# Kernel tuning notes

Measured on AMD Instinct MI355X. Metric: run time of the kernel, lower is better.

Reference implementation:

```python
import jax, jax.numpy as jnp
import numpy as np


def setup_inputs() -> dict:
    key = jax.random.key(0)
    k1, k2 = jax.random.split(key)
    b, feat = 8192, 256
    x = jax.random.normal(k1, (b, feat), dtype=jnp.float32)
    y = jax.random.randint(k2, (b,), 0, 100, dtype=jnp.int64)
    T = jnp.zeros((1,), dtype=jnp.float32)
    return {"x": x, "y": y, "T": T}


def reference(x, y, T):
    # SNNLoss.forward with inv=False, d=None, and no -1 labels in y
    b = x.shape[0]
    x = x / jnp.std(x, ddof=1)  # torch .std() is unbiased (ddof=1)

    # Pairwise Euclidean distance via Gram matrix (avoids [b,b,feat] blowup)
    sq = jnp.sum(x * x, axis=1)  # [b]
    d2 = jnp.maximum(sq[:, None] + sq[None, :] - 2.0 * (x @ x.T), 0.0)  # [b,b]
    eye = jnp.eye(b, dtype=bool)
    # diagonal is exactly 0 and masked out later; keep sqrt grad-safe there
    dist = jnp.where(eye, 0.0, jnp.sqrt(jnp.where(eye, 1.0, d2)))

    e_dist = -dist * jnp.power(jnp.float32(10.0), T[0])  # [b,b]
    neg_inf = jnp.float32(-jnp.inf)

    # denominator: all pairs except self
    den_dist = jnp.where(eye, neg_inf, e_dist)
    den = jax.scipy.special.logsumexp(den_dist, axis=1)  # [b]

    # numerator: same-label pairs except self
    m_num = (y[:, None] == y[None, :]) & ~eye  # [b,b]
    has = jnp.any(m_num, axis=1)  # rows with at least one positive
    num_dist = jnp.where(m_num, e_dist, neg_inf)
    # rows with no positives would give logsumexp = -inf; torch code zeroes
    # both num and den there. Substitute finite values, then zero the term.
    num = jax.scipy.special.logsumexp(jnp.where(has[:, None], num_dist, 0.0), axis=1)
    terms = jnp.where(has, num - den, 0.0)
    return -jnp.mean(terms)
```

## Files before the change

### kernel.cpp

```cpp
#include <hip/hip_runtime.h>

#define B_ROWS 8192
#define FEAT   256
#define NCH    8
#define CH_COLS 1024
#define NJT    16

typedef float f32x4 __attribute__((ext_vector_type(4)));
typedef _Float16 f16x8 __attribute__((ext_vector_type(8)));

typedef const __attribute__((address_space(1))) unsigned int* gas_ptr;
typedef __attribute__((address_space(3))) unsigned int* las_ptr;

__device__ __forceinline__ void gload_lds16(const void* g, void* l) {
  __builtin_amdgcn_global_load_lds((gas_ptr)g, (las_ptr)l, 16, 0, 0);
}

__global__ __launch_bounds__(256) void prep_kernel(
    const float* __restrict__ x, unsigned short* __restrict__ xh,
    float* __restrict__ sq, float* __restrict__ part_s,
    float* __restrict__ part_q)
{
  int tid = threadIdx.x;
  int l = tid & 63, wid = tid >> 6;
  int row = blockIdx.x * 4 + wid;
  const float4* xv = (const float4*)(x + (size_t)row * FEAT);
  float4 v = xv[l];
  ushort4 u;
  u.x = __builtin_bit_cast(unsigned short, (_Float16)v.x);
  u.y = __builtin_bit_cast(unsigned short, (_Float16)v.y);
  u.z = __builtin_bit_cast(unsigned short, (_Float16)v.z);
  u.w = __builtin_bit_cast(unsigned short, (_Float16)v.w);
  ((ushort4*)(xh + (size_t)row * FEAT))[l] = u;
  float ssq  = v.x*v.x + v.y*v.y + v.z*v.z + v.w*v.w;
  float ssum = v.x + v.y + v.z + v.w;
  #pragma unroll
  for (int m = 32; m; m >>= 1) {
    ssq  += __shfl_xor(ssq, m);
    ssum += __shfl_xor(ssum, m);
  }
  if (l == 0) sq[row] = ssq;
  __shared__ float red[8];
  if (l == 0) { red[wid*2] = ssum; red[wid*2+1] = ssq; }
  __syncthreads();
  if (tid == 0) {
    part_s[blockIdx.x] = red[0]+red[2]+red[4]+red[6];
    part_q[blockIdx.x] = red[1]+red[3]+red[5]+red[7];
  }
}

template<bool DIAG>
__device__ __forceinline__ void epilogue(
    const f32x4 (&acc)[2][4], const float* __restrict__ sq,
    const int* __restrict__ y, int j0, int l15,
    int i0q, const float (&sqi)[8], const int (&yiv)[8],
    float (&sden)[8], float (&snum)[8], float nscale2)
{
  int jb = j0 + l15;
  float sqj[4]; int yj[4];
  #pragma unroll
  for (int cb = 0; cb < 4; ++cb) {
    int j = jb + cb*16;
    sqj[cb] = sq[j];
    yj[cb]  = y[j];
  }
  #pragma unroll
  for (int rb = 0; rb < 2; ++rb) {
    #pragma unroll
    for (int r = 0; r < 4; ++r) {
      float si = sqi[rb*4+r];
      int   ig = i0q + rb*16 + r;
      int   yi = yiv[rb*4+r];
      float dacc = 0.f, nacc = 0.f;
      #pragma unroll
      for (int cb = 0; cb < 4; ++cb) {
        float S  = acc[rb][cb][r];
        float d2 = fmaf(S, -2.0f, si + sqj[cb]);
        d2 = fmaxf(d2, 0.0f);
        float e  = __builtin_amdgcn_exp2f(__builtin_amdgcn_sqrtf(d2) * nscale2);
        bool offd = !DIAG || (ig != jb + cb*16);
        dacc += offd ? e : 0.0f;
        nacc += (yi == yj[cb] && offd) ? e : 0.0f;
      }
      sden[rb*4+r] += dacc;
      snum[rb*4+r] += nacc;
    }
  }
}

__global__ __launch_bounds__(256, 2) void snn_main(
    const unsigned short* __restrict__ xh, const float* __restrict__ sq,
    const int* __restrict__ y, const float* __restrict__ T,
    const float* __restrict__ part_s, const float* __restrict__ part_q,
    float* __restrict__ pden, float* __restrict__ pnum)
{
  __shared__ __align__(16) char lB[32768];
  int tid = threadIdx.x;
  int l = tid & 63, wid = tid >> 6;
  int quad = l >> 4, l15 = l & 15;
  int l5 = l >> 5, s31 = l & 31;
  int ch = blockIdx.x, it = blockIdx.y;
  int i0 = it * 128, chbase = ch * CH_COLS;
  const char* xbc = (const char*)xh;

  f16x8 areg[2][8];
  #pragma unroll
  for (int rb = 0; rb < 2; ++rb)
    #pragma unroll
    for (int kk = 0; kk < 8; ++kk)
      areg[rb][kk] = *(const f16x8*)(xbc +
          (size_t)(i0 + wid*32 + rb*16 + l15)*512 + kk*64 + quad*16);

  float s_acc = 0.f, q_acc = 0.f;
  #pragma unroll
  for (int t = 0; t < 32; ++t) {
    s_acc += part_s[l + 64*t];
    q_acc += part_q[l + 64*t];
  }
  #pragma unroll
  for (int m = 1; m <= 32; m <<= 1) {
    s_acc += __shfl_xor(s_acc, m);
    q_acc += __shfl_xor(q_acc, m);
  }
  const double n = (double)B_ROWS * FEAT;
  double var = ((double)q_acc - (double)s_acc*(double)s_acc/n) / (n - 1.0);
  float stdv = (float)sqrt(var);
  float p10  = __builtin_amdgcn_exp2f(T[0] * 3.3219280948873623f);
  float nscale2 = -(p10 * 1.4426950408889634f / stdv);

  float sqi[8]; int yiv[8];
  int i0q = i0 + wid*32 + quad*4;
  #pragma unroll
  for (int rb = 0; rb < 2; ++rb)
    #pragma unroll
    for (int r = 0; r < 4; ++r) {
      int idx = i0q + rb*16 + r;
      sqi[rb*4+r] = sq[idx];
      yiv[rb*4+r] = y[idx];
    }

  float sden[8], snum[8];
  #pragma unroll
  for (int v = 0; v < 8; ++v) { sden[v] = 0.f; snum[v] = 0.f; }
  f32x4 acc[2][4];
  const f32x4 zero4 = {0.f, 0.f, 0.f, 0.f};

  for (int jt = 0; jt < NJT; ++jt) {
    int j0 = chbase + jt * 64;

    __syncthreads();
    {
      const char* gB = xbc + (size_t)j0 * 512;
      #pragma unroll
      for (int s = 0; s < 8; ++s) {
        int c  = wid*8 + s;
        int rw = 2*c + l5;
        int gg = s31 ^ (rw & 7);
        gload_lds16(gB + rw*512 + gg*16, lB + c*1024);
      }
    }

    if (jt > 0) {
      int pj0 = j0 - 64;
      if (pj0 == i0 || pj0 == i0 + 64)
        epilogue<true >(acc, sq, y, pj0, l15, i0q, sqi, yiv, sden, snum, nscale2);
      else
        epilogue<false>(acc, sq, y, pj0, l15, i0q, sqi, yiv, sden, snum, nscale2);
    }
    #pragma unroll
    for (int rb = 0; rb < 2; ++rb)
      #pragma unroll
      for (int cb = 0; cb < 4; ++cb)
        acc[rb][cb] = zero4;

    __syncthreads();

    #pragma unroll
    for (int kk = 0; kk < 8; ++kk) {
      f16x8 bv[4];
      #pragma unroll
      for (int cb = 0; cb < 4; ++cb) {
        int nr = cb*16 + l15;
        bv[cb] = *(const f16x8*)(lB + nr*512 + ((((kk<<2)|quad) ^ (l15 & 7)) << 4));
      }
      #pragma unroll
      for (int rb = 0; rb < 2; ++rb)
        #pragma unroll
        for (int cb = 0; cb < 4; ++cb)
          acc[rb][cb] = __builtin_amdgcn_mfma_f32_16x16x32_f16(areg[rb][kk], bv[cb], acc[rb][cb], 0, 0, 0);
    }
  }
  {
    int pj0 = chbase + (NJT-1) * 64;
    if (pj0 == i0 || pj0 == i0 + 64)
      epilogue<true >(acc, sq, y, pj0, l15, i0q, sqi, yiv, sden, snum, nscale2);
    else
      epilogue<false>(acc, sq, y, pj0, l15, i0q, sqi, yiv, sden, snum, nscale2);
  }

  #pragma unroll
  for (int v = 0; v < 8; ++v) {
    #pragma unroll
    for (int m = 1; m <= 8; m <<= 1) {
      sden[v] += __shfl_xor(sden[v], m);
      snum[v] += __shfl_xor(snum[v], m);
    }
  }
  if (l15 == 0) {
    int base = (it*NCH + ch) * 128;
    #pragma unroll
    for (int rb = 0; rb < 2; ++rb)
      #pragma unroll
      for (int r = 0; r < 4; ++r) {
        int rin = wid*32 + rb*16 + quad*4 + r;
        pden[base + rin] = sden[rb*4+r];
        pnum[base + rin] = snum[rb*4+r];
      }
  }
}

__global__ __launch_bounds__(1024) void final_kernel(
    const float* __restrict__ pden, const float* __restrict__ pnum,
    float* __restrict__ out)
{
  int tid = threadIdx.x;
  float tot = 0.f;
  #pragma unroll
  for (int rr = 0; rr < 8; ++rr) {
    int row = tid + 1024*rr;
    int itt = row >> 7, rin = row & 127;
    float den = 0.f, num = 0.f;
    #pragma unroll
    for (int p = 0; p < NCH; ++p) {
      den += pden[(itt*NCH + p)*128 + rin];
      num += pnum[(itt*NCH + p)*128 + rin];
    }
    if (num > 0.f)
      tot += 0.6931471805599453f *
             (__builtin_amdgcn_logf(num) - __builtin_amdgcn_logf(den));
  }
  #pragma unroll
  for (int m = 32; m; m >>= 1) tot += __shfl_xor(tot, m);
  __shared__ float red[16];
  if ((tid & 63) == 0) red[tid >> 6] = tot;
  __syncthreads();
  if (tid == 0) {
    float s = 0.f;
    #pragma unroll
    for (int w = 0; w < 16; ++w) s += red[w];
    out[0] = -s / 8192.0f;
  }
}

extern "C" void kernel_launch(void* const* d_in, const int* in_sizes, int n_in,
                              void* d_out, int out_size, void* d_ws, size_t ws_size,
                              hipStream_t stream)
{
  (void)in_sizes; (void)n_in; (void)out_size; (void)ws_size;
  const float* x  = (const float*)d_in[0];
  const int* y    = (const int*)d_in[1];
  const float* T  = (const float*)d_in[2];
  char* ws = (char*)d_ws;
  float* part_s = (float*)(ws + 1024);
  float* part_q = (float*)(ws + 1024 + 8192);
  float* sq     = (float*)(ws + 32768);
  unsigned short* xh = (unsigned short*)(ws + 65536);
  float* pden   = (float*)(ws + 65536 + 4194304);
  float* pnum   = pden + 64*NCH*128;

  hipLaunchKernelGGL(prep_kernel, dim3(B_ROWS/4), dim3(256), 0, stream,
                     x, xh, sq, part_s, part_q);
  hipLaunchKernelGGL(snn_main, dim3(NCH, B_ROWS/128), dim3(256), 0, stream,
                     xh, sq, y, T, part_s, part_q, pden, pnum);
  hipLaunchKernelGGL(final_kernel, dim3(1), dim3(1024), 0, stream,
                     pden, pnum, (float*)d_out);
}
```

Measured before the change: 120.8 us.

## Fuse prep, main and final kernels into one persistent kernel with grid barriers

Merges the conversion/statistics pass, the MFMA distance-and-exp pass and the final log reduction into a single 512-block kernel. Two software grid barriers built on atomics in workspace separate the phases. This removes two kernel launches and their inter-kernel gaps. In exchange it relies on all 512 blocks being co-resident, adds spin-wait cost at each barrier, and has a possible race between block 0 resetting the counters and other blocks arriving at the first barrier on repeated calls.

```diff
diff --git a/kernel.cpp b/kernel.cpp
--- a/kernel.cpp
+++ b/kernel.cpp
@@ -5,6 +5,8 @@
 #define NCH    8
 #define CH_COLS 1024
 #define NJT    16
+#define NBLK   512
+#define MAGIC  0x1357ACE5u
 
 typedef float f32x4 __attribute__((ext_vector_type(4)));
 typedef _Float16 f16x8 __attribute__((ext_vector_type(8)));
@@ -16,239 +18,280 @@
   __builtin_amdgcn_global_load_lds((gas_ptr)g, (las_ptr)l, 16, 0, 0);
 }
 
-__global__ __launch_bounds__(256) void prep_kernel(
-    const float* __restrict__ x, unsigned short* __restrict__ xh,
-    float* __restrict__ sq, float* __restrict__ part_s,
-    float* __restrict__ part_q)
-{
-  int tid = threadIdx.x;
-  int l = tid & 63, wid = tid >> 6;
-  int row = blockIdx.x * 4 + wid;
-  const float4* xv = (const float4*)(x + (size_t)row * FEAT);
-  float4 v = xv[l];
-  ushort4 u;
-  u.x = __builtin_bit_cast(unsigned short, (_Float16)v.x);
-  u.y = __builtin_bit_cast(unsigned short, (_Float16)v.y);
-  u.z = __builtin_bit_cast(unsigned short, (_Float16)v.z);
-  u.w = __builtin_bit_cast(unsigned short, (_Float16)v.w);
-  ((ushort4*)(xh + (size_t)row * FEAT))[l] = u;
-  float ssq  = v.x*v.x + v.y*v.y + v.z*v.z + v.w*v.w;
-  float ssum = v.x + v.y + v.z + v.w;
-  #pragma unroll
-  for (int m = 32; m; m >>= 1) {
-    ssq  += __shfl_xor(ssq, m);
-    ssum += __shfl_xor(ssum, m);
-  }
-  if (l == 0) sq[row] = ssq;
-  __shared__ float red[8];
-  if (l == 0) { red[wid*2] = ssum; red[wid*2+1] = ssq; }
+__device__ __forceinline__ void grid_barrier(unsigned* cnt) {
   __syncthreads();
-  if (tid == 0) {
-    part_s[blockIdx.x] = red[0]+red[2]+red[4]+red[6];
-    part_q[blockIdx.x] = red[1]+red[3]+red[5]+red[7];
-  }
+  if (threadIdx.x == 0) {
+    __threadfence();
+    atomicAdd(cnt, 1u);
+    while (__hip_atomic_load(cnt, __ATOMIC_ACQUIRE,
+                             __HIP_MEMORY_SCOPE_AGENT) < NBLK)
+      __builtin_amdgcn_s_sleep(1);
+  }
+  __syncthreads();
 }
 
-template<bool DIAG>
-__device__ __forceinline__ void epilogue(
-    const f32x4 (&acc)[2][4], const float* __restrict__ sq,
-    const int* __restrict__ y, int j0, int l15,
-    int i0q, const float (&sqi)[8], const int (&yiv)[8],
-    float (&sden)[8], float (&snum)[8], float nscale2)
-{
-  int jb = j0 + l15;
-  float sqj[4]; int yj[4];
-  #pragma unroll
-  for (int cb = 0; cb < 4; ++cb) {
-    int j = jb + cb*16;
-    sqj[cb] = sq[j];
-    yj[cb]  = y[j];
-  }
-  #pragma unroll
-  for (int rb = 0; rb < 2; ++rb) {
-    #pragma unroll
-    for (int r = 0; r < 4; ++r) {
-      float si = sqi[rb*4+r];
-      int   ig = i0q + rb*16 + r;
-      int   yi = yiv[rb*4+r];
-      float dacc = 0.f, nacc = 0.f;
-      #pragma unroll
-      for (int cb = 0; cb < 4; ++cb) {
-        float S  = acc[rb][cb][r];
-        float d2 = fmaf(S, -2.0f, si + sqj[cb]);
-        d2 = fmaxf(d2, 0.0f);
-        float e  = __builtin_amdgcn_exp2f(__builtin_amdgcn_sqrtf(d2) * nscale2);
-        bool offd = !DIAG || (ig != jb + cb*16);
-        dacc += offd ? e : 0.0f;
-        nacc += (yi == yj[cb] && offd) ? e : 0.0f;
-      }
-      sden[rb*4+r] += dacc;
-      snum[rb*4+r] += nacc;
-    }
-  }
-}
-
-__global__ __launch_bounds__(256, 2) void snn_main(
-    const unsigned short* __restrict__ xh, const float* __restrict__ sq,
-    const int* __restrict__ y, const float* __restrict__ T,
-    const float* __restrict__ part_s, const float* __restrict__ part_q,
-    float* __restrict__ pden, float* __restrict__ pnum)
+__global__ __launch_bounds__(256, 2) void snn_fused(
+    const float* __restrict__ x, const int* __restrict__ y,
+    const float* __restrict__ T,
+    unsigned* __restrict__ bar,
+    float* __restrict__ part_s, float* __restrict__ part_q,
+    float* __restrict__ sq, unsigned short* __restrict__ xh,
+    float* __restrict__ pden, float* __restrict__ pnum,
+    float* __restrict__ out)
 {
   __shared__ __align__(16) char lB[32768];
   int tid = threadIdx.x;
   int l = tid & 63, wid = tid >> 6;
   int quad = l >> 4, l15 = l & 15;
   int l5 = l >> 5, s31 = l & 31;
-  int ch = blockIdx.x, it = blockIdx.y;
+  int bid = blockIdx.x;
+  int ch = bid & 7, it = bid >> 3;
   int i0 = it * 128, chbase = ch * CH_COLS;
-  const char* xbc = (const char*)xh;
-
-  f16x8 areg[2][8];
-  #pragma unroll
-  for (int rb = 0; rb < 2; ++rb)
-    #pragma unroll
-    for (int kk = 0; kk < 8; ++kk)
-      areg[rb][kk] = *(const f16x8*)(xbc +
-          (size_t)(i0 + wid*32 + rb*16 + l15)*512 + kk*64 + quad*16);
-
-  float s_acc = 0.f, q_acc = 0.f;
-  #pragma unroll
-  for (int t = 0; t < 32; ++t) {
-    s_acc += part_s[l + 64*t];
-    q_acc += part_q[l + 64*t];
-  }
-  #pragma unroll
-  for (int m = 1; m <= 32; m <<= 1) {
-    s_acc += __shfl_xor(s_acc, m);
-    q_acc += __shfl_xor(q_acc, m);
-  }
-  const double n = (double)B_ROWS * FEAT;
-  double var = ((double)q_acc - (double)s_acc*(double)s_acc/n) / (n - 1.0);
-  float stdv = (float)sqrt(var);
-  float p10  = __builtin_amdgcn_exp2f(T[0] * 3.3219280948873623f);
-  float nscale2 = -(p10 * 1.4426950408889634f / stdv);
-
-  float sqi[8]; int yiv[8];
-  int i0q = i0 + wid*32 + quad*4;
-  #pragma unroll
-  for (int rb = 0; rb < 2; ++rb)
-    #pragma unroll
-    for (int r = 0; r < 4; ++r) {
-      int idx = i0q + rb*16 + r;
-      sqi[rb*4+r] = sq[idx];
-      yiv[rb*4+r] = y[idx];
-    }
-
-  float sden[8], snum[8];
-  #pragma unroll
-  for (int v = 0; v < 8; ++v) { sden[v] = 0.f; snum[v] = 0.f; }
-  f32x4 acc[2][4];
-  const f32x4 zero4 = {0.f, 0.f, 0.f, 0.f};
-
-  for (int jt = 0; jt < NJT; ++jt) {
-    int j0 = chbase + jt * 64;
-
+
+  if (bid == 0 && tid == 0) {
+    bar[0] = 0u; bar[1] = 0u;
+    __threadfence();
+    __hip_atomic_store(&bar[2], MAGIC, __ATOMIC_RELEASE,
+                       __HIP_MEMORY_SCOPE_AGENT);
+  }
+  if (tid == 0) {
+    while (__hip_atomic_load(&bar[2], __ATOMIC_ACQUIRE,
+                             __HIP_MEMORY_SCOPE_AGENT) != MAGIC)
+      __builtin_amdgcn_s_sleep(1);
+  }
+  __syncthreads();
+
+  {
+    float ls = 0.f, lq = 0.f;
+    #pragma unroll
+    for (int p = 0; p < 4; ++p) {
+      int row = bid*16 + p*4 + wid;
+      float4 v = ((const float4*)(x + (size_t)row * FEAT))[l];
+      ushort4 u;
+      u.x = __builtin_bit_cast(unsigned short, (_Float16)v.x);
+      u.y = __builtin_bit_cast(unsigned short, (_Float16)v.y);
+      u.z = __builtin_bit_cast(unsigned short, (_Float16)v.z);
+      u.w = __builtin_bit_cast(unsigned short, (_Float16)v.w);
+      ((ushort4*)(xh + (size_t)row * FEAT))[l] = u;
+      float q = v.x*v.x + v.y*v.y + v.z*v.z + v.w*v.w;
+      ls += v.x + v.y + v.z + v.w;
+      lq += q;
+      float rq = q;
+      #pragma unroll
+      for (int m = 32; m; m >>= 1) rq += __shfl_xor(rq, m);
+      if (l == 0) sq[row] = rq;
+    }
+    #pragma unroll
+    for (int m = 32; m; m >>= 1) {
+      ls += __shfl_xor(ls, m);
+      lq += __shfl_xor(lq, m);
+    }
+    __shared__ float red[8];
+    if (l == 0) { red[wid] = ls; red[4 + wid] = lq; }
     __syncthreads();
+    if (tid == 0) {
+      part_s[bid] = red[0]+red[1]+red[2]+red[3];
+      part_q[bid] = red[4]+red[5]+red[6]+red[7];
+    }
+  }
+
+  grid_barrier(&bar[0]);
+
+  {
+    const char* xbc = (const char*)xh;
+
+    f16x8 areg[2][8];
+    #pragma unroll
+    for (int rb = 0; rb < 2; ++rb)
+      #pragma unroll
+      for (int kk = 0; kk < 8; ++kk)
+        areg[rb][kk] = *(const f16x8*)(xbc +
+            (size_t)(i0 + wid*32 + rb*16 + l15)*512 + kk*64 + quad*16);
+
+    float s_acc = 0.f, q_acc = 0.f;
+    #pragma unroll
+    for (int t = 0; t < 8; ++t) {
+      s_acc += part_s[l + 64*t];
+      q_acc += part_q[l + 64*t];
+    }
+    #pragma unroll
+    for (int m = 1; m <= 32; m <<= 1) {
+      s_acc += __shfl_xor(s_acc, m);
+      q_acc += __shfl_xor(q_acc, m);
+    }
+    const double n = (double)B_ROWS * FEAT;
+    double var = ((double)q_acc - (double)s_acc*(double)s_acc/n) / (n - 1.0);
+    float stdv = (float)sqrt(var);
+    float p10  = __builtin_amdgcn_exp2f(T[0] * 3.3219280948873623f);
+    float nscale2 = -(p10 * 1.4426950408889634f / stdv);
+
+    float sqi[8]; int yiv[8];
+    int i0q = i0 + wid*32 + quad*4;
+    #pragma unroll
+    for (int rb = 0; rb < 2; ++rb)
+      #pragma unroll
+      for (int r = 0; r < 4; ++r) {
+        int idx = i0q + rb*16 + r;
+        sqi[rb*4+r] = sq[idx];
+        yiv[rb*4+r] = y[idx];
+      }
+
+    float sden[8], snum[8];
+    #pragma unroll
+    for (int v = 0; v < 8; ++v) { sden[v] = 0.f; snum[v] = 0.f; }
+    f32x4 acc[2][4];
+    const f32x4 zero4 = {0.f, 0.f, 0.f, 0.f};
+
+    for (int jt = 0; jt < NJT; ++jt) {
+      int j0 = chbase + jt * 64;
+
+      __syncthreads();
+      {
+        const char* gB = xbc + (size_t)j0 * 512;
+        #pragma unroll
+        for (int s = 0; s < 8; ++s) {
+          int c  = wid*8 + s;
+          int rw = 2*c + l5;
+          int gg = s31 ^ (rw & 7);
+          gload_lds16(gB + rw*512 + gg*16, lB + c*1024);
+        }
+      }
+
+      if (jt > 0) {
+        int pj0 = j0 - 64;
+        bool dg = (pj0 == i0 || pj0 == i0 + 64);
+        int jb = pj0 + l15;
+        float sqj[4]; int yj[4];
+        #pragma unroll
+        for (int cb = 0; cb < 4; ++cb) {
+          int j = jb + cb*16;
+          sqj[cb] = sq[j]; yj[cb] = y[j];
+        }
+        #pragma unroll
+        for (int rb = 0; rb < 2; ++rb)
+          #pragma unroll
+          for (int r = 0; r < 4; ++r) {
+            float si = sqi[rb*4+r];
+            int   ig = i0q + rb*16 + r;
+            int   yi = yiv[rb*4+r];
+            float dacc = 0.f, nacc = 0.f;
+            #pragma unroll
+            for (int cb = 0; cb < 4; ++cb) {
+              float S  = acc[rb][cb][r];
+              float d2 = fmaxf(fmaf(S, -2.0f, si + sqj[cb]), 0.0f);
+              float e  = __builtin_amdgcn_exp2f(
+                           __builtin_amdgcn_sqrtf(d2) * nscale2);
+              bool offd = !dg || (ig != jb + cb*16);
+              dacc += offd ? e : 0.0f;
+              nacc += (yi == yj[cb] && offd) ? e : 0.0f;
+            }
+            sden[rb*4+r] += dacc;
+            snum[rb*4+r] += nacc;
+          }
+      }
+      #pragma unroll
+      for (int rb = 0; rb < 2; ++rb)
+        #pragma unroll
+        for (int cb = 0; cb < 4; ++cb)
+          acc[rb][cb] = zero4;
+
+      __syncthreads();
+
+      #pragma unroll
+      for (int kk = 0; kk < 8; ++kk) {
+        f16x8 bv[4];
+        #pragma unroll
+        for (int cb = 0; cb < 4; ++cb) {
+          int nr = cb*16 + l15;
+          bv[cb] = *(const f16x8*)(lB + nr*512 +
+                     ((((kk<<2)|quad) ^ (l15 & 7)) << 4));
+        }
+        #pragma unroll
+        for (int rb = 0; rb < 2; ++rb)
+          #pragma unroll
+          for (int cb = 0; cb < 4; ++cb)
+            acc[rb][cb] = __builtin_amdgcn_mfma_f32_16x16x32_f16(
+                areg[rb][kk], bv[cb], acc[rb][cb], 0, 0, 0);
+      }
+    }
     {
-      const char* gB = xbc + (size_t)j0 * 512;
-      #pragma unroll
-      for (int s = 0; s < 8; ++s) {
-        int c  = wid*8 + s;
-        int rw = 2*c + l5;
-        int gg = s31 ^ (rw & 7);
-        gload_lds16(gB + rw*512 + gg*16, lB + c*1024);
-      }
-    }
-
-    if (jt > 0) {
-      int pj0 = j0 - 64;
-      if (pj0 == i0 || pj0 == i0 + 64)
-        epilogue<true >(acc, sq, y, pj0, l15, i0q, sqi, yiv, sden, snum, nscale2);
-      else
-        epilogue<false>(acc, sq, y, pj0, l15, i0q, sqi, yiv, sden, snum, nscale2);
-    }
-    #pragma unroll
-    for (int rb = 0; rb < 2; ++rb)
-      #pragma unroll
-      for (int cb = 0; cb < 4; ++cb)
-        acc[rb][cb] = zero4;
-
+      int pj0 = chbase + (NJT-1) * 64;
+      bool dg = (pj0 == i0 || pj0 == i0 + 64);
+      int jb = pj0 + l15;
+      float sqj[4]; int yj[4];
+      #pragma unroll
+      for (int cb = 0; cb < 4; ++cb) {
+        int j = jb + cb*16;
+        sqj[cb] = sq[j]; yj[cb] = y[j];
+      }
+      #pragma unroll
+      for (int rb = 0; rb < 2; ++rb)
+        #pragma unroll
+        for (int r = 0; r < 4; ++r) {
+          float si = sqi[rb*4+r];
+          int   ig = i0q + rb*16 + r;
+          int   yi = yiv[rb*4+r];
+          float dacc = 0.f, nacc = 0.f;
+          #pragma unroll
+          for (int cb = 0; cb < 4; ++cb) {
+            float S  = acc[rb][cb][r];
+            float d2 = fmaxf(fmaf(S, -2.0f, si + sqj[cb]), 0.0f);
+            float e  = __builtin_amdgcn_exp2f(
+                         __builtin_amdgcn_sqrtf(d2) * nscale2);
+            bool offd = !dg || (ig != jb + cb*16);
+            dacc += offd ? e : 0.0f;
+            nacc += (yi == yj[cb] && offd) ? e : 0.0f;
+          }
+          sden[rb*4+r] += dacc;
+          snum[rb*4+r] += nacc;
+        }
+    }
+
+    #pragma unroll
+    for (int v = 0; v < 8; ++v) {
+      #pragma unroll
+      for (int m = 1; m <= 8; m <<= 1) {
+        sden[v] += __shfl_xor(sden[v], m);
+        snum[v] += __shfl_xor(snum[v], m);
+      }
+    }
+    if (l15 == 0) {
+      int base = (it*NCH + ch) * 128;
+      #pragma unroll
+      for (int rb = 0; rb < 2; ++rb)
+        #pragma unroll
+        for (int r = 0; r < 4; ++r) {
+          int rin = wid*32 + rb*16 + quad*4 + r;
+          pden[base + rin] = sden[rb*4+r];
+          pnum[base + rin] = snum[rb*4+r];
+        }
+    }
+  }
+
+  grid_barrier(&bar[1]);
+
+  if (bid == 0) {
+    float tot = 0.f;
+    for (int k = 0; k < 32; ++k) {
+      int row = tid + 256*k;
+      int itt = row >> 7, rin = row & 127;
+      float den = 0.f, num = 0.f;
+      #pragma unroll
+      for (int p = 0; p < NCH; ++p) {
+        den += pden[(itt*NCH + p)*128 + rin];
+        num += pnum[(itt*NCH + p)*128 + rin];
+      }
+      if (num > 0.f)
+        tot += 0.6931471805599453f *
+               (__builtin_amdgcn_logf(num) - __builtin_amdgcn_logf(den));
+    }
+    #pragma unroll
+    for (int m = 32; m; m >>= 1) tot += __shfl_xor(tot, m);
+    __shared__ float fred[4];
+    if (l == 0) fred[wid] = tot;
     __syncthreads();
-
-    #pragma unroll
-    for (int kk = 0; kk < 8; ++kk) {
-      f16x8 bv[4];
-      #pragma unroll
-      for (int cb = 0; cb < 4; ++cb) {
-        int nr = cb*16 + l15;
-        bv[cb] = *(const f16x8*)(lB + nr*512 + ((((kk<<2)|quad) ^ (l15 & 7)) << 4));
-      }
-      #pragma unroll
-      for (int rb = 0; rb < 2; ++rb)
-        #pragma unroll
-        for (int cb = 0; cb < 4; ++cb)
-          acc[rb][cb] = __builtin_amdgcn_mfma_f32_16x16x32_f16(areg[rb][kk], bv[cb], acc[rb][cb], 0, 0, 0);
-    }
-  }
-  {
-    int pj0 = chbase + (NJT-1) * 64;
-    if (pj0 == i0 || pj0 == i0 + 64)
-      epilogue<true >(acc, sq, y, pj0, l15, i0q, sqi, yiv, sden, snum, nscale2);
-    else
-      epilogue<false>(acc, sq, y, pj0, l15, i0q, sqi, yiv, sden, snum, nscale2);
-  }
-
-  #pragma unroll
-  for (int v = 0; v < 8; ++v) {
-    #pragma unroll
-    for (int m = 1; m <= 8; m <<= 1) {
-      sden[v] += __shfl_xor(sden[v], m);
-      snum[v] += __shfl_xor(snum[v], m);
-    }
-  }
-  if (l15 == 0) {
-    int base = (it*NCH + ch) * 128;
-    #pragma unroll
-    for (int rb = 0; rb < 2; ++rb)
-      #pragma unroll
-      for (int r = 0; r < 4; ++r) {
-        int rin = wid*32 + rb*16 + quad*4 + r;
-        pden[base + rin] = sden[rb*4+r];
-        pnum[base + rin] = snum[rb*4+r];
-      }
-  }
-}
-
-__global__ __launch_bounds__(1024) void final_kernel(
-    const float* __restrict__ pden, const float* __restrict__ pnum,
-    float* __restrict__ out)
-{
-  int tid = threadIdx.x;
-  float tot = 0.f;
-  #pragma unroll
-  for (int rr = 0; rr < 8; ++rr) {
-    int row = tid + 1024*rr;
-    int itt = row >> 7, rin = row & 127;
-    float den = 0.f, num = 0.f;
-    #pragma unroll
-    for (int p = 0; p < NCH; ++p) {
-      den += pden[(itt*NCH + p)*128 + rin];
-      num += pnum[(itt*NCH + p)*128 + rin];
-    }
-    if (num > 0.f)
-      tot += 0.6931471805599453f *
-             (__builtin_amdgcn_logf(num) - __builtin_amdgcn_logf(den));
-  }
-  #pragma unroll
-  for (int m = 32; m; m >>= 1) tot += __shfl_xor(tot, m);
-  __shared__ float red[16];
-  if ((tid & 63) == 0) red[tid >> 6] = tot;
-  __syncthreads();
-  if (tid == 0) {
-    float s = 0.f;
-    #pragma unroll
-    for (int w = 0; w < 16; ++w) s += red[w];
-    out[0] = -s / 8192.0f;
+    if (tid == 0)
+      out[0] = -(fred[0]+fred[1]+fred[2]+fred[3]) / 8192.0f;
   }
 }
 
@@ -261,17 +304,15 @@
   const int* y    = (const int*)d_in[1];
   const float* T  = (const float*)d_in[2];
   char* ws = (char*)d_ws;
+  unsigned* bar = (unsigned*)ws;
   float* part_s = (float*)(ws + 1024);
-  float* part_q = (float*)(ws + 1024 + 8192);
+  float* part_q = (float*)(ws + 4096);
   float* sq     = (float*)(ws + 32768);
   unsigned short* xh = (unsigned short*)(ws + 65536);
   float* pden   = (float*)(ws + 65536 + 4194304);
   float* pnum   = pden + 64*NCH*128;
 
-  hipLaunchKernelGGL(prep_kernel, dim3(B_ROWS/4), dim3(256), 0, stream,
-                     x, xh, sq, part_s, part_q);
-  hipLaunchKernelGGL(snn_main, dim3(NCH, B_ROWS/128), dim3(256), 0, stream,
-                     xh, sq, y, T, part_s, part_q, pden, pnum);
-  hipLaunchKernelGGL(final_kernel, dim3(1), dim3(1024), 0, stream,
+  hipLaunchKernelGGL(snn_fused, dim3(NBLK), dim3(256), 0, stream,
+                     x, y, T, bar, part_s, part_q, sq, xh,
                      pden, pnum, (float*)d_out);
 }
```

After: 232.1 us. 92.2% more time.

## Exploit distance symmetry by computing only upper-triangular 128x128 tile pairs

Applied to the files above, without the earlier changes.

Replaces the full 8192x8192 sweep with 2080 upper-triangular 128x128 tile pairs. Each off-diagonal tile contributes both row and column partial sums of exp(-dist), which roughly halves the MFMA and exp/sqrt work. Partial sums are reduced in LDS and then accumulated with global float atomics into per-row den/num buffers that the prep kernel zeroes. The cost is 128KB of dynamic LDS per block (so likely one block per CU), a non-pipelined load-then-compute structure, atomic contention, and summation order that varies between runs.

```diff
diff --git a/kernel.cpp b/kernel.cpp
--- a/kernel.cpp
+++ b/kernel.cpp
@@ -2,28 +2,21 @@
 
 #define B_ROWS 8192
 #define FEAT   256
-#define NCH    8
-#define CH_COLS 1024
-#define NJT    16
+#define NPAIR  2080
+#define TILE_B 65536
 
 typedef float f32x4 __attribute__((ext_vector_type(4)));
 typedef _Float16 f16x8 __attribute__((ext_vector_type(8)));
-
-typedef const __attribute__((address_space(1))) unsigned int* gas_ptr;
-typedef __attribute__((address_space(3))) unsigned int* las_ptr;
-
-__device__ __forceinline__ void gload_lds16(const void* g, void* l) {
-  __builtin_amdgcn_global_load_lds((gas_ptr)g, (las_ptr)l, 16, 0, 0);
-}
 
 __global__ __launch_bounds__(256) void prep_kernel(
     const float* __restrict__ x, unsigned short* __restrict__ xh,
     float* __restrict__ sq, float* __restrict__ part_s,
-    float* __restrict__ part_q)
+    float* __restrict__ part_q, float* __restrict__ gden)
 {
   int tid = threadIdx.x;
   int l = tid & 63, wid = tid >> 6;
   int row = blockIdx.x * 4 + wid;
+  if (blockIdx.x < 64) gden[blockIdx.x * 256 + tid] = 0.f;
   const float4* xv = (const float4*)(x + (size_t)row * FEAT);
   float4 v = xv[l];
   ushort4 u;
@@ -49,67 +42,55 @@
   }
 }
 
-template<bool DIAG>
-__device__ __forceinline__ void epilogue(
-    const f32x4 (&acc)[2][4], const float* __restrict__ sq,
-    const int* __restrict__ y, int j0, int l15,
-    int i0q, const float (&sqi)[8], const int (&yiv)[8],
-    float (&sden)[8], float (&snum)[8], float nscale2)
-{
-  int jb = j0 + l15;
-  float sqj[4]; int yj[4];
-  #pragma unroll
-  for (int cb = 0; cb < 4; ++cb) {
-    int j = jb + cb*16;
-    sqj[cb] = sq[j];
-    yj[cb]  = y[j];
-  }
-  #pragma unroll
-  for (int rb = 0; rb < 2; ++rb) {
-    #pragma unroll
-    for (int r = 0; r < 4; ++r) {
-      float si = sqi[rb*4+r];
-      int   ig = i0q + rb*16 + r;
-      int   yi = yiv[rb*4+r];
-      float dacc = 0.f, nacc = 0.f;
-      #pragma unroll
-      for (int cb = 0; cb < 4; ++cb) {
-        float S  = acc[rb][cb][r];
-        float d2 = fmaf(S, -2.0f, si + sqj[cb]);
-        d2 = fmaxf(d2, 0.0f);
-        float e  = __builtin_amdgcn_exp2f(__builtin_amdgcn_sqrtf(d2) * nscale2);
-        bool offd = !DIAG || (ig != jb + cb*16);
-        dacc += offd ? e : 0.0f;
-        nacc += (yi == yj[cb] && offd) ? e : 0.0f;
-      }
-      sden[rb*4+r] += dacc;
-      snum[rb*4+r] += nacc;
-    }
-  }
-}
-
-__global__ __launch_bounds__(256, 2) void snn_main(
+__global__ __launch_bounds__(512, 2) void snn_main(
     const unsigned short* __restrict__ xh, const float* __restrict__ sq,
     const int* __restrict__ y, const float* __restrict__ T,
     const float* __restrict__ part_s, const float* __restrict__ part_q,
-    float* __restrict__ pden, float* __restrict__ pnum)
-{
-  __shared__ __align__(16) char lB[32768];
+    float* __restrict__ gden, float* __restrict__ gnum)
+{
+  extern __shared__ char smem[];
+  char* lA = smem;
+  char* lB = smem + TILE_B;
   int tid = threadIdx.x;
-  int l = tid & 63, wid = tid >> 6;
+  int l = tid & 63, w = tid >> 6;
   int quad = l >> 4, l15 = l & 15;
-  int l5 = l >> 5, s31 = l & 31;
-  int ch = blockIdx.x, it = blockIdx.y;
-  int i0 = it * 128, chbase = ch * CH_COLS;
+  int wr = w >> 1, wc = w & 1;
+
+  int p = blockIdx.x;
+  int ti = (int)((129.0 - sqrt(129.0*129.0 - 8.0*(double)p)) * 0.5);
+  while ((ti+1)*(129-(ti+1))/2 <= p) ++ti;
+  while (ti*(129-ti)/2 > p) --ti;
+  int tj = ti + (p - ti*(129-ti)/2);
+  bool diag = (ti == tj);
+  int i0 = ti*128, j0 = tj*128;
+
   const char* xbc = (const char*)xh;
-
-  f16x8 areg[2][8];
-  #pragma unroll
-  for (int rb = 0; rb < 2; ++rb)
-    #pragma unroll
-    for (int kk = 0; kk < 8; ++kk)
-      areg[rb][kk] = *(const f16x8*)(xbc +
-          (size_t)(i0 + wid*32 + rb*16 + l15)*512 + kk*64 + quad*16);
+  {
+    const uint4* gA = (const uint4*)(xbc + (size_t)i0*512);
+    uint4 ta[8], tb[8];
+    #pragma unroll
+    for (int s = 0; s < 8; ++s) ta[s] = gA[s*512 + tid];
+    if (!diag) {
+      const uint4* gB = (const uint4*)(xbc + (size_t)j0*512);
+      #pragma unroll
+      for (int s = 0; s < 8; ++s) tb[s] = gB[s*512 + tid];
+    }
+    #pragma unroll
+    for (int s = 0; s < 8; ++s) {
+      int ll = s*512 + tid;
+      int rw = ll >> 5, g = ll & 31;
+      *(uint4*)(lA + rw*512 + ((g ^ (rw & 7)) << 4)) = ta[s];
+    }
+    if (!diag) {
+      #pragma unroll
+      for (int s = 0; s < 8; ++s) {
+        int ll = s*512 + tid;
+        int rw = ll >> 5, g = ll & 31;
+        *(uint4*)(lB + rw*512 + ((g ^ (rw & 7)) << 4)) = tb[s];
+      }
+    }
+  }
+  const char* lBr = diag ? lA : lB;
 
   float s_acc = 0.f, q_acc = 0.f;
   #pragma unroll
@@ -129,98 +110,126 @@
   float nscale2 = -(p10 * 1.4426950408889634f / stdv);
 
   float sqi[8]; int yiv[8];
-  int i0q = i0 + wid*32 + quad*4;
   #pragma unroll
   for (int rb = 0; rb < 2; ++rb)
     #pragma unroll
-    for (int r = 0; r < 4; ++r) {
-      int idx = i0q + rb*16 + r;
-      sqi[rb*4+r] = sq[idx];
-      yiv[rb*4+r] = y[idx];
-    }
-
-  float sden[8], snum[8];
-  #pragma unroll
-  for (int v = 0; v < 8; ++v) { sden[v] = 0.f; snum[v] = 0.f; }
+    for (int rr = 0; rr < 4; ++rr) {
+      int i = i0 + wr*32 + rb*16 + quad*4 + rr;
+      sqi[rb*4+rr] = sq[i]; yiv[rb*4+rr] = y[i];
+    }
+  float sqj[4]; int yjv[4];
+  #pragma unroll
+  for (int cb = 0; cb < 4; ++cb) {
+    int j = j0 + wc*64 + cb*16 + l15;
+    sqj[cb] = sq[j]; yjv[cb] = y[j];
+  }
+
   f32x4 acc[2][4];
-  const f32x4 zero4 = {0.f, 0.f, 0.f, 0.f};
-
-  for (int jt = 0; jt < NJT; ++jt) {
-    int j0 = chbase + jt * 64;
-
-    __syncthreads();
-    {
-      const char* gB = xbc + (size_t)j0 * 512;
-      #pragma unroll
-      for (int s = 0; s < 8; ++s) {
-        int c  = wid*8 + s;
-        int rw = 2*c + l5;
-        int gg = s31 ^ (rw & 7);
-        gload_lds16(gB + rw*512 + gg*16, lB + c*1024);
+  const f32x4 zero4 = {0.f,0.f,0.f,0.f};
+  #pragma unroll
+  for (int rb = 0; rb < 2; ++rb)
+    #pragma unroll
+    for (int cb = 0; cb < 4; ++cb) acc[rb][cb] = zero4;
+
+  __syncthreads();
+
+  #pragma unroll
+  for (int kk = 0; kk < 8; ++kk) {
+    f16x8 av[2], bv[4];
+    #pragma unroll
+    for (int rb = 0; rb < 2; ++rb) {
+      int m = wr*32 + rb*16 + l15;
+      av[rb] = *(const f16x8*)(lA + m*512 + ((((kk<<2)|quad) ^ (l15 & 7)) << 4));
+    }
+    #pragma unroll
+    for (int cb = 0; cb < 4; ++cb) {
+      int nr = wc*64 + cb*16 + l15;
+      bv[cb] = *(const f16x8*)(lBr + nr*512 + ((((kk<<2)|quad) ^ (l15 & 7)) << 4));
+    }
+    #pragma unroll
+    for (int rb = 0; rb < 2; ++rb)
+      #pragma unroll
+      for (int cb = 0; cb < 4; ++cb)
+        acc[rb][cb] = __builtin_amdgcn_mfma_f32_16x16x32_f16(av[rb], bv[cb], acc[rb][cb], 0, 0, 0);
+  }
+
+  float rden[8], rnum[8], cden[4], cnum[4];
+  #pragma unroll
+  for (int v = 0; v < 8; ++v) { rden[v] = 0.f; rnum[v] = 0.f; }
+  #pragma unroll
+  for (int v = 0; v < 4; ++v) { cden[v] = 0.f; cnum[v] = 0.f; }
+
+  #pragma unroll
+  for (int rb = 0; rb < 2; ++rb) {
+    #pragma unroll
+    for (int rr = 0; rr < 4; ++rr) {
+      int ig = i0 + wr*32 + rb*16 + quad*4 + rr;
+      float si = sqi[rb*4+rr];
+      int   yi = yiv[rb*4+rr];
+      #pragma unroll
+      for (int cb = 0; cb < 4; ++cb) {
+        int jg = j0 + wc*64 + cb*16 + l15;
+        float S  = acc[rb][cb][rr];
+        float d2 = fmaxf(fmaf(S, -2.0f, si + sqj[cb]), 0.0f);
+        float e  = __builtin_amdgcn_exp2f(__builtin_amdgcn_sqrtf(d2) * nscale2);
+        if (diag && ig == jg) e = 0.0f;
+        bool same = (yi == yjv[cb]);
+        rden[rb*4+rr] += e;
+        rnum[rb*4+rr] += same ? e : 0.0f;
+        cden[cb] += e;
+        cnum[cb] += same ? e : 0.0f;
       }
     }
-
-    if (jt > 0) {
-      int pj0 = j0 - 64;
-      if (pj0 == i0 || pj0 == i0 + 64)
-        epilogue<true >(acc, sq, y, pj0, l15, i0q, sqi, yiv, sden, snum, nscale2);
-      else
-        epilogue<false>(acc, sq, y, pj0, l15, i0q, sqi, yiv, sden, snum, nscale2);
-    }
+  }
+
+  #pragma unroll
+  for (int v = 0; v < 8; ++v) {
+    #pragma unroll
+    for (int m = 1; m <= 8; m <<= 1) {
+      rden[v] += __shfl_xor(rden[v], m);
+      rnum[v] += __shfl_xor(rnum[v], m);
+    }
+  }
+  #pragma unroll
+  for (int v = 0; v < 4; ++v) {
+    cden[v] += __shfl_xor(cden[v], 16); cden[v] += __shfl_xor(cden[v], 32);
+    cnum[v] += __shfl_xor(cnum[v], 16); cnum[v] += __shfl_xor(cnum[v], 32);
+  }
+
+  __syncthreads();
+  float* red = (float*)smem;
+  red[tid] = 0.f;
+  __syncthreads();
+  if (l15 == 0) {
+    int rbase = wr*32 + quad*4;
     #pragma unroll
     for (int rb = 0; rb < 2; ++rb)
       #pragma unroll
-      for (int cb = 0; cb < 4; ++cb)
-        acc[rb][cb] = zero4;
-
-    __syncthreads();
-
-    #pragma unroll
-    for (int kk = 0; kk < 8; ++kk) {
-      f16x8 bv[4];
-      #pragma unroll
-      for (int cb = 0; cb < 4; ++cb) {
-        int nr = cb*16 + l15;
-        bv[cb] = *(const f16x8*)(lB + nr*512 + ((((kk<<2)|quad) ^ (l15 & 7)) << 4));
+      for (int rr = 0; rr < 4; ++rr) {
+        atomicAdd(&red[      rbase + rb*16 + rr], rden[rb*4+rr]);
+        atomicAdd(&red[128 + rbase + rb*16 + rr], rnum[rb*4+rr]);
       }
-      #pragma unroll
-      for (int rb = 0; rb < 2; ++rb)
-        #pragma unroll
-        for (int cb = 0; cb < 4; ++cb)
-          acc[rb][cb] = __builtin_amdgcn_mfma_f32_16x16x32_f16(areg[rb][kk], bv[cb], acc[rb][cb], 0, 0, 0);
-    }
-  }
-  {
-    int pj0 = chbase + (NJT-1) * 64;
-    if (pj0 == i0 || pj0 == i0 + 64)
-      epilogue<true >(acc, sq, y, pj0, l15, i0q, sqi, yiv, sden, snum, nscale2);
-    else
-      epilogue<false>(acc, sq, y, pj0, l15, i0q, sqi, yiv, sden, snum, nscale2);
-  }
-
-  #pragma unroll
-  for (int v = 0; v < 8; ++v) {
-    #pragma unroll
-    for (int m = 1; m <= 8; m <<= 1) {
-      sden[v] += __shfl_xor(sden[v], m);
-      snum[v] += __shfl_xor(snum[v], m);
-    }
-  }
-  if (l15 == 0) {
-    int base = (it*NCH + ch) * 128;
-    #pragma unroll
-    for (int rb = 0; rb < 2; ++rb)
-      #pragma unroll
-      for (int r = 0; r < 4; ++r) {
-        int rin = wid*32 + rb*16 + quad*4 + r;
-        pden[base + rin] = sden[rb*4+r];
-        pnum[base + rin] = snum[rb*4+r];
-      }
+  }
+  if (!diag && quad == 0) {
+    #pragma unroll
+    for (int cb = 0; cb < 4; ++cb) {
+      int c = wc*64 + cb*16 + l15;
+      atomicAdd(&red[256 + c], cden[cb]);
+      atomicAdd(&red[384 + c], cnum[cb]);
+    }
+  }
+  __syncthreads();
+  if (tid < 256) {
+    int r = tid & 127;
+    atomicAdd((tid < 128 ? gden : gnum) + i0 + r, red[tid]);
+  } else if (!diag) {
+    int r = tid & 127;
+    atomicAdd((tid < 384 ? gden : gnum) + j0 + r, red[tid]);
   }
 }
 
 __global__ __launch_bounds__(1024) void final_kernel(
-    const float* __restrict__ pden, const float* __restrict__ pnum,
+    const float* __restrict__ gden, const float* __restrict__ gnum,
     float* __restrict__ out)
 {
   int tid = threadIdx.x;
@@ -228,13 +237,7 @@
   #pragma unroll
   for (int rr = 0; rr < 8; ++rr) {
     int row = tid + 1024*rr;
-    int itt = row >> 7, rin = row & 127;
-    float den = 0.f, num = 0.f;
-    #pragma unroll
-    for (int p = 0; p < NCH; ++p) {
-      den += pden[(itt*NCH + p)*128 + rin];
-      num += pnum[(itt*NCH + p)*128 + rin];
-    }
+    float den = gden[row], num = gnum[row];
     if (num > 0.f)
       tot += 0.6931471805599453f *
              (__builtin_amdgcn_logf(num) - __builtin_amdgcn_logf(den));
@@ -265,13 +268,15 @@
   float* part_q = (float*)(ws + 1024 + 8192);
   float* sq     = (float*)(ws + 32768);
   unsigned short* xh = (unsigned short*)(ws + 65536);
-  float* pden   = (float*)(ws + 65536 + 4194304);
-  float* pnum   = pden + 64*NCH*128;
+  float* gden   = (float*)(ws + 65536 + 4194304);
+  float* gnum   = gden + 8192;
 
   hipLaunchKernelGGL(prep_kernel, dim3(B_ROWS/4), dim3(256), 0, stream,
-                     x, xh, sq, part_s, part_q);
-  hipLaunchKernelGGL(snn_main, dim3(NCH, B_ROWS/128), dim3(256), 0, stream,
-                     xh, sq, y, T, part_s, part_q, pden, pnum);
+                     x, xh, sq, part_s, part_q, gden);
+  hipFuncSetAttribute((const void*)snn_main,
+                      hipFuncAttributeMaxDynamicSharedMemorySize, 2*TILE_B);
+  hipLaunchKernelGGL(snn_main, dim3(NPAIR), dim3(512), 2*TILE_B, stream,
+                     xh, sq, y, T, part_s, part_q, gden, gnum);
   hipLaunchKernelGGL(final_kernel, dim3(1), dim3(1024), 0, stream,
-                     pden, pnum, (float*)d_out);
-}
+                     gden, gnum, (float*)d_out);
+}
```

Result: slower. 193.8 us (+60.5%).
